# Performance work log

Hardware: AMD Instinct MI355X
Metric: run time of the kernel (lower is better)

The kernel has to match this reference:

```python
import jax, jax.numpy as jnp
import numpy as np

D_MODEL = 1024
N_HEADS = 16
HEAD_DIM = D_MODEL // N_HEADS
B, S = 4, 2048


def setup_inputs() -> dict:
    key = jax.random.key(0)
    ks = jax.random.split(key, 11)
    scale = 1.0 / np.sqrt(D_MODEL)
    inp = {
        "query": jax.random.normal(ks[0], (B, S, D_MODEL), jnp.float32),
        "key": jax.random.normal(ks[1], (B, S, D_MODEL), jnp.float32),
        "value": jax.random.normal(ks[2], (B, S, D_MODEL), jnp.float32),
        "Wq": jax.random.normal(ks[3], (D_MODEL, D_MODEL), jnp.float32) * scale,
        "bq": jnp.zeros((D_MODEL,), jnp.float32),
        "Wk": jax.random.normal(ks[4], (D_MODEL, D_MODEL), jnp.float32) * scale,
        "bk": jnp.zeros((D_MODEL,), jnp.float32),
        "Wv": jax.random.normal(ks[5], (D_MODEL, D_MODEL), jnp.float32) * scale,
        "bv": jnp.zeros((D_MODEL,), jnp.float32),
        "Wo": jax.random.normal(ks[6], (D_MODEL, D_MODEL), jnp.float32) * scale,
        "bo": jnp.zeros((D_MODEL,), jnp.float32),
    }
    return inp


def _split_heads(x):
    b, s, _ = x.shape
    return x.reshape(b, s, N_HEADS, HEAD_DIM).transpose(0, 2, 1, 3)  # b h s d


def reference(query, key, value, Wq, bq, Wk, bk, Wv, bv, Wo, bo):
    Q = _split_heads(query @ Wq.T + bq)
    K = _split_heads(key @ Wk.T + bk)
    V = _split_heads(value @ Wv.T + bv)
    scale = 1.0 / jnp.sqrt(jnp.float32(HEAD_DIM))
    energy = jnp.einsum("bhqd,bhkd->bhqk", Q, K) * scale  # full N x N scores
    attn = jax.nn.softmax(energy, axis=-1)
    x = jnp.einsum("bhqk,bhkd->bhqd", attn, V)
    x = x.transpose(0, 2, 1, 3).reshape(query.shape[0], -1, D_MODEL)
    return x @ Wo.T + bo
```

## Files before the change

### kernel.cpp

```cpp
#include <hip/hip_runtime.h>
#include <cstdint>
#include <cstddef>


typedef unsigned short u16;
typedef unsigned u32;
typedef short short8 __attribute__((ext_vector_type(8)));
typedef __bf16 bf16x8 __attribute__((ext_vector_type(8)));
typedef float f32x4 __attribute__((ext_vector_type(4)));
typedef float f32x16 __attribute__((ext_vector_type(16)));
typedef unsigned short u16x4 __attribute__((ext_vector_type(4)));
typedef unsigned u32x2 __attribute__((ext_vector_type(2)));
typedef unsigned u32x4 __attribute__((ext_vector_type(4)));
typedef int iv2 __attribute__((ext_vector_type(2)));

__device__ __forceinline__ u16 f2bf(float f) {
  unsigned u = __builtin_bit_cast(unsigned, f);
  u += 0x7fffu + ((u >> 16) & 1u);
  return (u16)(u >> 16);
}
__device__ __forceinline__ bf16x8 bc8(short8 v) { return __builtin_bit_cast(bf16x8, v); }
__device__ __forceinline__ u32 pk_bf16(float a, float b) {
  u32 r;
  asm("v_cvt_pk_bf16_f32 %0, %1, %2" : "=v"(r) : "v"(a), "v"(b));
  return r;
}
__device__ __forceinline__ void gload16(const u16* g, u16* l) {
  __builtin_amdgcn_global_load_lds((const __attribute__((address_space(1))) void*)g,
                                   (__attribute__((address_space(3))) void*)l, 16, 0, 0);
}

__global__ __launch_bounds__(256) void cvt_all(const float* __restrict__ q,
                                               const float* __restrict__ k,
                                               const float* __restrict__ v,
                                               const float* __restrict__ wq,
                                               const float* __restrict__ wk,
                                               const float* __restrict__ wv,
                                               const float* __restrict__ wo,
                                               u16* __restrict__ xq, u16* __restrict__ xk,
                                               u16* __restrict__ xv, u16* __restrict__ wqb,
                                               u16* __restrict__ wkb, u16* __restrict__ wvb,
                                               u16* __restrict__ wob) {
  const size_t i4 = (size_t)blockIdx.x * 256 + threadIdx.x;
  const size_t A4 = 1ull << 21, W4 = 1ull << 18;
  const float* s;
  u16* d;
  size_t off;
  if (i4 < 3 * A4) {
    const int r = (int)(i4 >> 21);
    off = i4 & (A4 - 1);
    s = r == 0 ? q : (r == 1 ? k : v);
    d = r == 0 ? xq : (r == 1 ? xk : xv);
  } else {
    const size_t t = i4 - 3 * A4;
    const int r = (int)(t >> 18);
    off = t & (W4 - 1);
    s = r == 0 ? wq : (r == 1 ? wk : (r == 2 ? wv : wo));
    d = r == 0 ? wqb : (r == 1 ? wkb : (r == 2 ? wvb : wob));
  }
  const f32x4 a = ((const f32x4*)s)[off];
  u32x2 o = {pk_bf16(a[0], a[1]), pk_bf16(a[2], a[3])};
  ((u32x2*)d)[off] = o;
}

template <int MODE>
__device__ __forceinline__ void gemm_core(u16* lA, u16* lB,
                                          const u16* __restrict__ A,
                                          const u16* __restrict__ Bw,
                                          const float* __restrict__ bias,
                                          void* __restrict__ C, float oscale,
                                          int M, int N, int K) {
  const int tid = threadIdx.x;
  const int w = tid >> 6, l = tid & 63, g = l >> 4, m = l & 15;
  const int wr = w >> 1, wc = w & 1;
  const int m0 = blockIdx.y * 128, n0 = blockIdx.x * 128;

  const int j0 = w * 2, j1 = w * 2 + 1;
  const int r0 = j0 * 16 + (l >> 2), r1 = j1 * 16 + (l >> 2);
  const int sc8 = (l & 3) * 8;
  const u16* gA0 = A + (size_t)(m0 + r0) * K + sc8;
  const u16* gA1 = A + (size_t)(m0 + r1) * K + sc8;
  const u16* gB0 = Bw + (size_t)(n0 + r0) * K + sc8;
  const u16* gB1 = Bw + (size_t)(n0 + r1) * K + sc8;
  u16* lA0 = lA + j0 * 512;
  u16* lA1 = lA + j1 * 512;
  u16* lB0 = lB + j0 * 512;
  u16* lB1 = lB + j1 * 512;

  f32x4 acc[4][4];
  const f32x4 z = {0.f, 0.f, 0.f, 0.f};
#pragma unroll
  for (int i = 0; i < 4; ++i)
#pragma unroll
    for (int j = 0; j < 4; ++j) acc[i][j] = z;

  const int nk = K >> 5;
  for (int kk = 0; kk < nk; ++kk) {
    const int ko = kk * 32;
    gload16(gA0 + ko, lA0);
    gload16(gA1 + ko, lA1);
    gload16(gB0 + ko, lB0);
    gload16(gB1 + ko, lB1);
    __syncthreads();
    bf16x8 af[4], bf2[4];
#pragma unroll
    for (int i = 0; i < 4; ++i)
      af[i] = bc8(*(const short8*)(lA + (wr * 64 + i * 16 + m) * 32 + g * 8));
#pragma unroll
    for (int j = 0; j < 4; ++j)
      bf2[j] = bc8(*(const short8*)(lB + (wc * 64 + j * 16 + m) * 32 + g * 8));
#pragma unroll
    for (int i = 0; i < 4; ++i)
#pragma unroll
      for (int j = 0; j < 4; ++j)
        acc[i][j] = __builtin_amdgcn_mfma_f32_16x16x32_bf16(af[i], bf2[j], acc[i][j], 0, 0, 0);
    __syncthreads();
  }

  float bv[4];
#pragma unroll
  for (int j = 0; j < 4; ++j) bv[j] = bias[n0 + wc * 64 + j * 16 + m];

  if (MODE == 2) {
#pragma unroll
    for (int i = 0; i < 4; ++i)
#pragma unroll
      for (int j = 0; j < 4; ++j) {
        const int row0 = m0 + wr * 64 + i * 16 + g * 4;
        const int col = n0 + wc * 64 + j * 16 + m;
        u16x4 o;
#pragma unroll
        for (int r = 0; r < 4; ++r) o[r] = f2bf((acc[i][j][r] + bv[j]) * oscale);
        *(u16x4*)((u16*)C + ((size_t)(row0 >> 11) * 1024 + col) * 2048 + (row0 & 2047)) = o;
      }
  } else {
#pragma unroll
    for (int i = 0; i < 4; ++i) {
#pragma unroll
      for (int r = 0; r < 4; ++r) {
        const int row = m0 + wr * 64 + i * 16 + g * 4 + r;
#pragma unroll
        for (int j = 0; j < 4; ++j) {
          const int col = n0 + wc * 64 + j * 16 + m;
          const float v = (acc[i][j][r] + bv[j]) * oscale;
          if (MODE == 0)
            ((float*)C)[(size_t)row * N + col] = v;
          else
            ((u16*)C)[(size_t)row * N + col] = f2bf(v);
        }
      }
    }
  }
}

__global__ __launch_bounds__(256) void qk_gemm(const u16* __restrict__ xq,
                                               const u16* __restrict__ xk,
                                               const u16* __restrict__ wqb,
                                               const u16* __restrict__ wkb,
                                               const float* __restrict__ bq,
                                               const float* __restrict__ bk,
                                               u16* __restrict__ Qp, u16* __restrict__ Kp,
                                               float SC) {
  __shared__ alignas(16) u16 lA[128 * 32];
  __shared__ alignas(16) u16 lB[128 * 32];
  const int z = blockIdx.z;
  gemm_core<1>(lA, lB, z ? xk : xq, z ? wkb : wqb, z ? bk : bq,
               z ? (void*)Kp : (void*)Qp, z ? 1.f : SC, 8192, 1024, 1024);
}

__global__ __launch_bounds__(256) void v_gemm(const u16* __restrict__ xv,
                                              const u16* __restrict__ wvb,
                                              const float* __restrict__ bv,
                                              u16* __restrict__ Vt) {
  __shared__ alignas(16) u16 lA[128 * 32];
  __shared__ alignas(16) u16 lB[128 * 32];
  gemm_core<2>(lA, lB, xv, wvb, bv, Vt, 1.f, 8192, 1024, 1024);
}

__global__ __launch_bounds__(256) void o_gemm(const u16* __restrict__ Xa,
                                              const u16* __restrict__ wob,
                                              const float* __restrict__ bo,
                                              float* __restrict__ out) {
  __shared__ alignas(16) u16 lA[128 * 32];
  __shared__ alignas(16) u16 lB[128 * 32];
  gemm_core<0>(lA, lB, Xa, wob, bo, out, 1.f, 8192, 1024, 1024);
}

__global__ __launch_bounds__(512, 4) void attn_fwd(const u16* __restrict__ Q,
                                                   const u16* __restrict__ Kp,
                                                   const u16* __restrict__ Vt,
                                                   u16* __restrict__ Xa) {
  __shared__ alignas(16) u16 kl[64][72];
  __shared__ alignas(16) u16 vl[64][72];
  const int tid = threadIdx.x;
  const int l = tid & 63, w = tid >> 6;
  const int q32 = l & 31, hi = l >> 5;
  const int lin = blockIdx.x + 8 * blockIdx.y;
  const int xp = lin >> 6, yp = lin & 63;
  const int b = yp >> 4, h = yp & 15;
  const int q0 = xp * 256 + w * 32;

  bf16x8 qf[4];
  const size_t qrow = (size_t)b * 2048 + q0 + q32;
#pragma unroll
  for (int ds = 0; ds < 4; ++ds)
    qf[ds] = bc8(*(const short8*)(Q + qrow * 1024 + h * 64 + ds * 16 + hi * 8));

  f32x16 of[2] = {{}, {}};
  float l0 = 0.f, l1 = 0.f, l2 = 0.f, l3 = 0.f;

  const int sr = tid >> 3;
  const int sc8 = (tid & 7) * 8;
  const u16* Kb = Kp + (size_t)b * 2048 * 1024 + h * 64;
  const u16* Vb = Vt + (size_t)yp * 64 * 2048;

  short8 rk = *(const short8*)(Kb + (size_t)sr * 1024 + sc8);
  short8 rv = *(const short8*)(Vb + (size_t)sr * 2048 + sc8);

  for (int kt = 0; kt < 32; ++kt) {
    *(short8*)(&kl[sr][sc8]) = rk;
    *(short8*)(&vl[sr][sc8]) = rv;
    __syncthreads();
    if (kt + 1 < 32) {
      rk = *(const short8*)(Kb + (size_t)((kt + 1) * 64 + sr) * 1024 + sc8);
      rv = *(const short8*)(Vb + (size_t)sr * 2048 + (kt + 1) * 64 + sc8);
    }

#pragma unroll
    for (int kt2 = 0; kt2 < 2; ++kt2) {
      f32x16 st = {};
#pragma unroll
      for (int ds = 0; ds < 4; ++ds) {
        const bf16x8 kf = bc8(*(const short8*)(&kl[kt2 * 32 + q32][ds * 16 + hi * 8]));
        st = __builtin_amdgcn_mfma_f32_32x32x16_bf16(kf, qf[ds], st, 0, 0, 0);
      }
      float p[16];
#pragma unroll
      for (int r = 0; r < 16; ++r) p[r] = __builtin_amdgcn_exp2f(st[r]);
      l0 += (p[0] + p[1]) + (p[2] + p[3]);
      l1 += (p[4] + p[5]) + (p[6] + p[7]);
      l2 += (p[8] + p[9]) + (p[10] + p[11]);
      l3 += (p[12] + p[13]) + (p[14] + p[15]);
#pragma unroll
      for (int s = 0; s < 2; ++s) {
        int X0 = (int)pk_bf16(p[8 * s + 0], p[8 * s + 1]);
        int X1 = (int)pk_bf16(p[8 * s + 2], p[8 * s + 3]);
        int Y0 = (int)pk_bf16(p[8 * s + 4], p[8 * s + 5]);
        int Y1 = (int)pk_bf16(p[8 * s + 6], p[8 * s + 7]);
        iv2 r0 = __builtin_amdgcn_permlane32_swap(X0, Y0, false, false);
        iv2 r1 = __builtin_amdgcn_permlane32_swap(X1, Y1, false, false);
        u32x4 bw = {(u32)r0[0], (u32)r1[0], (u32)r0[1], (u32)r1[1]};
        const bf16x8 pb = __builtin_bit_cast(bf16x8, bw);
        const int ks = kt2 * 2 + s;
#pragma unroll
        for (int dt = 0; dt < 2; ++dt) {
          const bf16x8 vf = bc8(*(const short8*)(&vl[dt * 32 + q32][ks * 16 + hi * 8]));
          of[dt] = __builtin_amdgcn_mfma_f32_32x32x16_bf16(vf, pb, of[dt], 0, 0, 0);
        }
      }
    }
    __syncthreads();
  }

  float lo = (l0 + l1) + (l2 + l3);
  lo += __shfl_xor(lo, 32, 64);
  const float inv = 1.0f / lo;

#pragma unroll
  for (int dt = 0; dt < 2; ++dt)
#pragma unroll
    for (int rg = 0; rg < 4; ++rg) {
      u32x2 o2;
      o2[0] = pk_bf16(of[dt][4 * rg + 0] * inv, of[dt][4 * rg + 1] * inv);
      o2[1] = pk_bf16(of[dt][4 * rg + 2] * inv, of[dt][4 * rg + 3] * inv);
      *(u32x2*)(Xa + qrow * 1024 + h * 64 + dt * 32 + rg * 8 + hi * 4) = o2;
    }
}

extern "C" void kernel_launch(void* const* d_in, const int* in_sizes, int n_in,
                              void* d_out, int out_size, void* d_ws, size_t ws_size,
                              hipStream_t stream) {
  const float* q  = (const float*)d_in[0];
  const float* k  = (const float*)d_in[1];
  const float* v  = (const float*)d_in[2];
  const float* Wq = (const float*)d_in[3];
  const float* bq = (const float*)d_in[4];
  const float* Wk = (const float*)d_in[5];
  const float* bk = (const float*)d_in[6];
  const float* Wv = (const float*)d_in[7];
  const float* bv = (const float*)d_in[8];
  const float* Wo = (const float*)d_in[9];
  const float* bo = (const float*)d_in[10];

  char* ws = (char*)d_ws;
  const size_t MB = 1024ull * 1024ull;
  u16* wqb = (u16*)(ws + 0 * MB);
  u16* wkb = (u16*)(ws + 2 * MB);
  u16* wvb = (u16*)(ws + 4 * MB);
  u16* wob = (u16*)(ws + 6 * MB);
  u16* xq  = (u16*)(ws + 8 * MB);
  u16* xk  = (u16*)(ws + 24 * MB);
  u16* xv  = (u16*)(ws + 40 * MB);
  u16* Qp  = (u16*)(ws + 56 * MB);
  u16* Kp  = (u16*)(ws + 72 * MB);
  u16* Vt  = xk;
  u16* Xa  = xq;

  cvt_all<<<28672, 256, 0, stream>>>(q, k, v, Wq, Wk, Wv, Wo,
                                     xq, xk, xv, wqb, wkb, wvb, wob);

  const float SC = 0.125f * 1.44269504f;
  qk_gemm<<<dim3(8, 64, 2), 256, 0, stream>>>(xq, xk, wqb, wkb, bq, bk, Qp, Kp, SC);
  v_gemm<<<dim3(8, 64), 256, 0, stream>>>(xv, wvb, bv, Vt);

  attn_fwd<<<dim3(8, 64), 512, 0, stream>>>(Qp, Kp, Vt, Xa);

  o_gemm<<<dim3(8, 64), 256, 0, stream>>>(Xa, wob, bo, (float*)d_out);
}
```

Measured before the change: 224.8 us.

## Fuse fp32-to-bf16 activation conversion into QKV projection GEMM loads

Drops the separate pass that converted the q/k/v activations to bf16. The projection GEMM now loads fp32 tiles straight into LDS using an XOR-swizzled layout and packs them to bf16 while reading fragments. The Q, K and V projections are merged into one launch with a z dimension of 3, and block indices are remapped to group tiles. This removes one full write and re-read of the 48MB activation buffers and one launch, at the cost of twice the A-tile global/LDS traffic inside the GEMM plus conversion ALU work in the inner loop.

```diff
diff --git a/kernel.cpp b/kernel.cpp
--- a/kernel.cpp
+++ b/kernel.cpp
@@ -29,63 +29,68 @@
   __builtin_amdgcn_global_load_lds((const __attribute__((address_space(1))) void*)g,
                                    (__attribute__((address_space(3))) void*)l, 16, 0, 0);
 }
-
-__global__ __launch_bounds__(256) void cvt_all(const float* __restrict__ q,
-                                               const float* __restrict__ k,
-                                               const float* __restrict__ v,
-                                               const float* __restrict__ wq,
-                                               const float* __restrict__ wk,
-                                               const float* __restrict__ wv,
-                                               const float* __restrict__ wo,
-                                               u16* __restrict__ xq, u16* __restrict__ xk,
-                                               u16* __restrict__ xv, u16* __restrict__ wqb,
-                                               u16* __restrict__ wkb, u16* __restrict__ wvb,
-                                               u16* __restrict__ wob) {
+__device__ __forceinline__ void gload16f(const float* g, float* l) {
+  __builtin_amdgcn_global_load_lds((const __attribute__((address_space(1))) void*)g,
+                                   (__attribute__((address_space(3))) void*)l, 16, 0, 0);
+}
+
+__global__ __launch_bounds__(256) void cvt_w(const float* __restrict__ wq,
+                                             const float* __restrict__ wk,
+                                             const float* __restrict__ wv,
+                                             const float* __restrict__ wo,
+                                             u16* __restrict__ wqb, u16* __restrict__ wkb,
+                                             u16* __restrict__ wvb, u16* __restrict__ wob) {
   const size_t i4 = (size_t)blockIdx.x * 256 + threadIdx.x;
-  const size_t A4 = 1ull << 21, W4 = 1ull << 18;
-  const float* s;
-  u16* d;
-  size_t off;
-  if (i4 < 3 * A4) {
-    const int r = (int)(i4 >> 21);
-    off = i4 & (A4 - 1);
-    s = r == 0 ? q : (r == 1 ? k : v);
-    d = r == 0 ? xq : (r == 1 ? xk : xv);
-  } else {
-    const size_t t = i4 - 3 * A4;
-    const int r = (int)(t >> 18);
-    off = t & (W4 - 1);
-    s = r == 0 ? wq : (r == 1 ? wk : (r == 2 ? wv : wo));
-    d = r == 0 ? wqb : (r == 1 ? wkb : (r == 2 ? wvb : wob));
-  }
+  const size_t W4 = 1ull << 18;
+  const int r = (int)(i4 >> 18);
+  const size_t off = i4 & (W4 - 1);
+  const float* s = r == 0 ? wq : (r == 1 ? wk : (r == 2 ? wv : wo));
+  u16* d = r == 0 ? wqb : (r == 1 ? wkb : (r == 2 ? wvb : wob));
   const f32x4 a = ((const f32x4*)s)[off];
   u32x2 o = {pk_bf16(a[0], a[1]), pk_bf16(a[2], a[3])};
   ((u32x2*)d)[off] = o;
 }
 
-template <int MODE>
-__device__ __forceinline__ void gemm_core(u16* lA, u16* lB,
-                                          const u16* __restrict__ A,
+template <int AF32>
+__device__ __forceinline__ void gemm_core(char* lds, const void* __restrict__ A,
                                           const u16* __restrict__ Bw,
                                           const float* __restrict__ bias,
-                                          void* __restrict__ C, float oscale,
-                                          int M, int N, int K) {
+                                          void* __restrict__ C, int mode, float oscale) {
+  constexpr int K = 1024, N = 1024;
   const int tid = threadIdx.x;
   const int w = tid >> 6, l = tid & 63, g = l >> 4, m = l & 15;
   const int wr = w >> 1, wc = w & 1;
-  const int m0 = blockIdx.y * 128, n0 = blockIdx.x * 128;
+  const int lin = blockIdx.x + 8 * blockIdx.y;
+  const int xp = lin >> 6, yp = lin & 63;
+  const int m0 = yp * 128, n0 = xp * 128;
+
+  float* lAf = (float*)lds;
+  u16* lA = (u16*)lds;
+  u16* lB = (u16*)(lds + (AF32 ? 16384 : 8192));
 
   const int j0 = w * 2, j1 = w * 2 + 1;
-  const int r0 = j0 * 16 + (l >> 2), r1 = j1 * 16 + (l >> 2);
-  const int sc8 = (l & 3) * 8;
-  const u16* gA0 = A + (size_t)(m0 + r0) * K + sc8;
-  const u16* gA1 = A + (size_t)(m0 + r1) * K + sc8;
-  const u16* gB0 = Bw + (size_t)(n0 + r0) * K + sc8;
-  const u16* gB1 = Bw + (size_t)(n0 + r1) * K + sc8;
-  u16* lA0 = lA + j0 * 512;
-  u16* lA1 = lA + j1 * 512;
-  u16* lB0 = lB + j0 * 512;
-  u16* lB1 = lB + j1 * 512;
+  const int br0 = j0 * 16 + (l >> 2), br1 = j1 * 16 + (l >> 2);
+  const int bcol = (l & 3) * 8;
+  const u16* gB0 = Bw + (size_t)(n0 + br0) * K + bcol;
+  const u16* gB1 = Bw + (size_t)(n0 + br1) * K + bcol;
+
+  const u16 *gA0 = nullptr, *gA1 = nullptr;
+  const float* gAf[4];
+  float* lAd[4];
+  if constexpr (AF32) {
+    const float* Af = (const float*)A;
+    const int acol = ((l & 7) ^ (l >> 3)) * 4;
+#pragma unroll
+    for (int cc = 0; cc < 4; ++cc) {
+      const int c = w * 4 + cc;
+      gAf[cc] = Af + (size_t)(m0 + c * 8 + (l >> 3)) * K + acol;
+      lAd[cc] = lAf + c * 256;
+    }
+  } else {
+    const u16* Ab = (const u16*)A;
+    gA0 = Ab + (size_t)(m0 + br0) * K + bcol;
+    gA1 = Ab + (size_t)(m0 + br1) * K + bcol;
+  }
 
   f32x4 acc[4][4];
   const f32x4 z = {0.f, 0.f, 0.f, 0.f};
@@ -94,26 +99,43 @@
 #pragma unroll
     for (int j = 0; j < 4; ++j) acc[i][j] = z;
 
-  const int nk = K >> 5;
-  for (int kk = 0; kk < nk; ++kk) {
+  for (int kk = 0; kk < 32; ++kk) {
     const int ko = kk * 32;
-    gload16(gA0 + ko, lA0);
-    gload16(gA1 + ko, lA1);
-    gload16(gB0 + ko, lB0);
-    gload16(gB1 + ko, lB1);
+    if constexpr (AF32) {
+#pragma unroll
+      for (int cc = 0; cc < 4; ++cc) gload16f(gAf[cc] + ko, lAd[cc]);
+    } else {
+      gload16(gA0 + ko, lA + j0 * 512);
+      gload16(gA1 + ko, lA + j1 * 512);
+    }
+    gload16(gB0 + ko, lB + j0 * 512);
+    gload16(gB1 + ko, lB + j1 * 512);
     __syncthreads();
-    bf16x8 af[4], bf2[4];
+
+    bf16x8 af[4], bfr[4];
+#pragma unroll
+    for (int i = 0; i < 4; ++i) {
+      if constexpr (AF32) {
+        const int base = (wr * 64 + i * 16 + m) * 32;
+        const int G0 = ((2 * g) ^ (m & 7)) * 4;
+        const int G1 = ((2 * g + 1) ^ (m & 7)) * 4;
+        const f32x4 lo = *(const f32x4*)(lAf + base + G0);
+        const f32x4 hi = *(const f32x4*)(lAf + base + G1);
+        u32x4 wd = {pk_bf16(lo[0], lo[1]), pk_bf16(lo[2], lo[3]),
+                    pk_bf16(hi[0], hi[1]), pk_bf16(hi[2], hi[3])};
+        af[i] = __builtin_bit_cast(bf16x8, wd);
+      } else {
+        af[i] = bc8(*(const short8*)(lA + (wr * 64 + i * 16 + m) * 32 + g * 8));
+      }
+    }
+#pragma unroll
+    for (int j = 0; j < 4; ++j)
+      bfr[j] = bc8(*(const short8*)(lB + (wc * 64 + j * 16 + m) * 32 + g * 8));
 #pragma unroll
     for (int i = 0; i < 4; ++i)
-      af[i] = bc8(*(const short8*)(lA + (wr * 64 + i * 16 + m) * 32 + g * 8));
-#pragma unroll
-    for (int j = 0; j < 4; ++j)
-      bf2[j] = bc8(*(const short8*)(lB + (wc * 64 + j * 16 + m) * 32 + g * 8));
-#pragma unroll
-    for (int i = 0; i < 4; ++i)
 #pragma unroll
       for (int j = 0; j < 4; ++j)
-        acc[i][j] = __builtin_amdgcn_mfma_f32_16x16x32_bf16(af[i], bf2[j], acc[i][j], 0, 0, 0);
+        acc[i][j] = __builtin_amdgcn_mfma_f32_16x16x32_bf16(af[i], bfr[j], acc[i][j], 0, 0, 0);
     __syncthreads();
   }
 
@@ -121,7 +143,7 @@
 #pragma unroll
   for (int j = 0; j < 4; ++j) bv[j] = bias[n0 + wc * 64 + j * 16 + m];
 
-  if (MODE == 2) {
+  if (mode == 2) {
 #pragma unroll
     for (int i = 0; i < 4; ++i)
 #pragma unroll
@@ -143,7 +165,7 @@
         for (int j = 0; j < 4; ++j) {
           const int col = n0 + wc * 64 + j * 16 + m;
           const float v = (acc[i][j][r] + bv[j]) * oscale;
-          if (MODE == 0)
+          if (mode == 0)
             ((float*)C)[(size_t)row * N + col] = v;
           else
             ((u16*)C)[(size_t)row * N + col] = f2bf(v);
@@ -153,37 +175,32 @@
   }
 }
 
-__global__ __launch_bounds__(256) void qk_gemm(const u16* __restrict__ xq,
-                                               const u16* __restrict__ xk,
-                                               const u16* __restrict__ wqb,
-                                               const u16* __restrict__ wkb,
-                                               const float* __restrict__ bq,
-                                               const float* __restrict__ bk,
-                                               u16* __restrict__ Qp, u16* __restrict__ Kp,
-                                               float SC) {
-  __shared__ alignas(16) u16 lA[128 * 32];
-  __shared__ alignas(16) u16 lB[128 * 32];
+__global__ __launch_bounds__(256) void qkv_gemm(const float* __restrict__ q,
+                                                const float* __restrict__ k,
+                                                const float* __restrict__ v,
+                                                const u16* __restrict__ wqb,
+                                                const u16* __restrict__ wkb,
+                                                const u16* __restrict__ wvb,
+                                                const float* __restrict__ bq,
+                                                const float* __restrict__ bk,
+                                                const float* __restrict__ bv,
+                                                u16* __restrict__ Qp, u16* __restrict__ Kp,
+                                                u16* __restrict__ Vt, float SC) {
+  __shared__ alignas(16) char lds[24576];
   const int z = blockIdx.z;
-  gemm_core<1>(lA, lB, z ? xk : xq, z ? wkb : wqb, z ? bk : bq,
-               z ? (void*)Kp : (void*)Qp, z ? 1.f : SC, 8192, 1024, 1024);
-}
-
-__global__ __launch_bounds__(256) void v_gemm(const u16* __restrict__ xv,
-                                              const u16* __restrict__ wvb,
-                                              const float* __restrict__ bv,
-                                              u16* __restrict__ Vt) {
-  __shared__ alignas(16) u16 lA[128 * 32];
-  __shared__ alignas(16) u16 lB[128 * 32];
-  gemm_core<2>(lA, lB, xv, wvb, bv, Vt, 1.f, 8192, 1024, 1024);
+  const float* A = z == 0 ? q : (z == 1 ? k : v);
+  const u16* W = z == 0 ? wqb : (z == 1 ? wkb : wvb);
+  const float* bi = z == 0 ? bq : (z == 1 ? bk : bv);
+  void* C = z == 0 ? (void*)Qp : (z == 1 ? (void*)Kp : (void*)Vt);
+  gemm_core<1>(lds, A, W, bi, C, z == 2 ? 2 : 1, z == 0 ? SC : 1.f);
 }
 
 __global__ __launch_bounds__(256) void o_gemm(const u16* __restrict__ Xa,
                                               const u16* __restrict__ wob,
                                               const float* __restrict__ bo,
                                               float* __restrict__ out) {
-  __shared__ alignas(16) u16 lA[128 * 32];
-  __shared__ alignas(16) u16 lB[128 * 32];
-  gemm_core<0>(lA, lB, Xa, wob, bo, out, 1.f, 8192, 1024, 1024);
+  __shared__ alignas(16) char lds[16384];
+  gemm_core<0>(lds, Xa, wob, bo, out, 0, 1.f);
 }
 
 __global__ __launch_bounds__(512, 4) void attn_fwd(const u16* __restrict__ Q,
@@ -298,20 +315,16 @@
   u16* wkb = (u16*)(ws + 2 * MB);
   u16* wvb = (u16*)(ws + 4 * MB);
   u16* wob = (u16*)(ws + 6 * MB);
-  u16* xq  = (u16*)(ws + 8 * MB);
-  u16* xk  = (u16*)(ws + 24 * MB);
-  u16* xv  = (u16*)(ws + 40 * MB);
-  u16* Qp  = (u16*)(ws + 56 * MB);
-  u16* Kp  = (u16*)(ws + 72 * MB);
-  u16* Vt  = xk;
-  u16* Xa  = xq;
-
-  cvt_all<<<28672, 256, 0, stream>>>(q, k, v, Wq, Wk, Wv, Wo,
-                                     xq, xk, xv, wqb, wkb, wvb, wob);
+  u16* Qp  = (u16*)(ws + 8 * MB);
+  u16* Kp  = (u16*)(ws + 24 * MB);
+  u16* Vt  = (u16*)(ws + 40 * MB);
+  u16* Xa  = (u16*)(ws + 56 * MB);
+
+  cvt_w<<<4096, 256, 0, stream>>>(Wq, Wk, Wv, Wo, wqb, wkb, wvb, wob);
 
   const float SC = 0.125f * 1.44269504f;
-  qk_gemm<<<dim3(8, 64, 2), 256, 0, stream>>>(xq, xk, wqb, wkb, bq, bk, Qp, Kp, SC);
-  v_gemm<<<dim3(8, 64), 256, 0, stream>>>(xv, wvb, bv, Vt);
+  qkv_gemm<<<dim3(8, 64, 3), 256, 0, stream>>>(q, k, v, wqb, wkb, wvb,
+                                               bq, bk, bv, Qp, Kp, Vt, SC);
 
   attn_fwd<<<dim3(8, 64), 512, 0, stream>>>(Qp, Kp, Vt, Xa);
 
```

New measurement: 230.1 us. 2.4% more time.

## Double-buffer GEMM LDS, use 512-thread blocks, fuse QKV projections into one launch

Applied to the files above, without the earlier changes.

The projection GEMM core now keeps two LDS stages, so the global-to-LDS load for the next K slice is issued before the MFMAs on the current slice. That removes one barrier per iteration and overlaps memory with compute. Blocks grow to 8 waves, each computing a 32x64 sub-tile, and block indices are remapped so that consecutive blocks share row tiles for better L2 reuse. The Q, K and V GEMMs merge into one launch with z=3, and Vt moves to its own workspace region so it no longer aliases xk, which the same launch still reads. The cost is a larger LDS footprint and less register-level reuse per wave.

```diff
diff --git a/kernel.cpp b/kernel.cpp
--- a/kernel.cpp
+++ b/kernel.cpp
@@ -63,57 +63,57 @@
   ((u32x2*)d)[off] = o;
 }
 
-template <int MODE>
-__device__ __forceinline__ void gemm_core(u16* lA, u16* lB,
-                                          const u16* __restrict__ A,
+__device__ __forceinline__ void gemm_core(u16* lds, const u16* __restrict__ A,
                                           const u16* __restrict__ Bw,
                                           const float* __restrict__ bias,
-                                          void* __restrict__ C, float oscale,
-                                          int M, int N, int K) {
+                                          void* __restrict__ C, int mode, float oscale) {
+  constexpr int K = 1024, N = 1024;
   const int tid = threadIdx.x;
   const int w = tid >> 6, l = tid & 63, g = l >> 4, m = l & 15;
-  const int wr = w >> 1, wc = w & 1;
-  const int m0 = blockIdx.y * 128, n0 = blockIdx.x * 128;
-
-  const int j0 = w * 2, j1 = w * 2 + 1;
-  const int r0 = j0 * 16 + (l >> 2), r1 = j1 * 16 + (l >> 2);
-  const int sc8 = (l & 3) * 8;
-  const u16* gA0 = A + (size_t)(m0 + r0) * K + sc8;
-  const u16* gA1 = A + (size_t)(m0 + r1) * K + sc8;
-  const u16* gB0 = Bw + (size_t)(n0 + r0) * K + sc8;
-  const u16* gB1 = Bw + (size_t)(n0 + r1) * K + sc8;
-  u16* lA0 = lA + j0 * 512;
-  u16* lA1 = lA + j1 * 512;
-  u16* lB0 = lB + j0 * 512;
-  u16* lB1 = lB + j1 * 512;
-
-  f32x4 acc[4][4];
+  const int wr = w & 3, wc = w >> 2;
+  const int lin = blockIdx.x + 8 * blockIdx.y;
+  const int xp = lin >> 6, yp = lin & 63;
+  const int m0 = yp * 128, n0 = xp * 128;
+
+  const int srow = w * 16 + (l >> 2);
+  const int scol = (l & 3) * 8;
+  const u16* gA = A + (size_t)(m0 + srow) * K + scol;
+  const u16* gB = Bw + (size_t)(n0 + srow) * K + scol;
+  u16* lA[2] = {lds + 0, lds + 8192};
+  u16* lB[2] = {lds + 4096, lds + 12288};
+  u16* dstA[2] = {lA[0] + w * 512, lA[1] + w * 512};
+  u16* dstB[2] = {lB[0] + w * 512, lB[1] + w * 512};
+
+  f32x4 acc[2][4];
   const f32x4 z = {0.f, 0.f, 0.f, 0.f};
 #pragma unroll
-  for (int i = 0; i < 4; ++i)
+  for (int i = 0; i < 2; ++i)
 #pragma unroll
     for (int j = 0; j < 4; ++j) acc[i][j] = z;
 
-  const int nk = K >> 5;
-  for (int kk = 0; kk < nk; ++kk) {
-    const int ko = kk * 32;
-    gload16(gA0 + ko, lA0);
-    gload16(gA1 + ko, lA1);
-    gload16(gB0 + ko, lB0);
-    gload16(gB1 + ko, lB1);
-    __syncthreads();
-    bf16x8 af[4], bf2[4];
-#pragma unroll
-    for (int i = 0; i < 4; ++i)
-      af[i] = bc8(*(const short8*)(lA + (wr * 64 + i * 16 + m) * 32 + g * 8));
+  gload16(gA, dstA[0]);
+  gload16(gB, dstB[0]);
+  __syncthreads();
+
+  for (int kk = 0; kk < 32; ++kk) {
+    const int cur = kk & 1, nxt = cur ^ 1;
+    if (kk + 1 < 32) {
+      const int ko = (kk + 1) * 32;
+      gload16(gA + ko, dstA[nxt]);
+      gload16(gB + ko, dstB[nxt]);
+    }
+    bf16x8 af[2], bfr[4];
+#pragma unroll
+    for (int i = 0; i < 2; ++i)
+      af[i] = bc8(*(const short8*)(lA[cur] + (wr * 32 + i * 16 + m) * 32 + g * 8));
 #pragma unroll
     for (int j = 0; j < 4; ++j)
-      bf2[j] = bc8(*(const short8*)(lB + (wc * 64 + j * 16 + m) * 32 + g * 8));
-#pragma unroll
-    for (int i = 0; i < 4; ++i)
+      bfr[j] = bc8(*(const short8*)(lB[cur] + (wc * 64 + j * 16 + m) * 32 + g * 8));
+#pragma unroll
+    for (int i = 0; i < 2; ++i)
 #pragma unroll
       for (int j = 0; j < 4; ++j)
-        acc[i][j] = __builtin_amdgcn_mfma_f32_16x16x32_bf16(af[i], bf2[j], acc[i][j], 0, 0, 0);
+        acc[i][j] = __builtin_amdgcn_mfma_f32_16x16x32_bf16(af[i], bfr[j], acc[i][j], 0, 0, 0);
     __syncthreads();
   }
 
@@ -121,12 +121,12 @@
 #pragma unroll
   for (int j = 0; j < 4; ++j) bv[j] = bias[n0 + wc * 64 + j * 16 + m];
 
-  if (MODE == 2) {
-#pragma unroll
-    for (int i = 0; i < 4; ++i)
+  if (mode == 2) {
+#pragma unroll
+    for (int i = 0; i < 2; ++i)
 #pragma unroll
       for (int j = 0; j < 4; ++j) {
-        const int row0 = m0 + wr * 64 + i * 16 + g * 4;
+        const int row0 = m0 + wr * 32 + i * 16 + g * 4;
         const int col = n0 + wc * 64 + j * 16 + m;
         u16x4 o;
 #pragma unroll
@@ -135,15 +135,15 @@
       }
   } else {
 #pragma unroll
-    for (int i = 0; i < 4; ++i) {
+    for (int i = 0; i < 2; ++i) {
 #pragma unroll
       for (int r = 0; r < 4; ++r) {
-        const int row = m0 + wr * 64 + i * 16 + g * 4 + r;
+        const int row = m0 + wr * 32 + i * 16 + g * 4 + r;
 #pragma unroll
         for (int j = 0; j < 4; ++j) {
           const int col = n0 + wc * 64 + j * 16 + m;
           const float v = (acc[i][j][r] + bv[j]) * oscale;
-          if (MODE == 0)
+          if (mode == 0)
             ((float*)C)[(size_t)row * N + col] = v;
           else
             ((u16*)C)[(size_t)row * N + col] = f2bf(v);
@@ -153,37 +153,32 @@
   }
 }
 
-__global__ __launch_bounds__(256) void qk_gemm(const u16* __restrict__ xq,
-                                               const u16* __restrict__ xk,
-                                               const u16* __restrict__ wqb,
-                                               const u16* __restrict__ wkb,
-                                               const float* __restrict__ bq,
-                                               const float* __restrict__ bk,
-                                               u16* __restrict__ Qp, u16* __restrict__ Kp,
-                                               float SC) {
-  __shared__ alignas(16) u16 lA[128 * 32];
-  __shared__ alignas(16) u16 lB[128 * 32];
+__global__ __launch_bounds__(512, 2) void qkv_gemm(const u16* __restrict__ xq,
+                                                   const u16* __restrict__ xk,
+                                                   const u16* __restrict__ xv,
+                                                   const u16* __restrict__ wqb,
+                                                   const u16* __restrict__ wkb,
+                                                   const u16* __restrict__ wvb,
+                                                   const float* __restrict__ bq,
+                                                   const float* __restrict__ bk,
+                                                   const float* __restrict__ bv,
+                                                   u16* __restrict__ Qp, u16* __restrict__ Kp,
+                                                   u16* __restrict__ Vt, float SC) {
+  __shared__ alignas(16) u16 lds[16384];
   const int z = blockIdx.z;
-  gemm_core<1>(lA, lB, z ? xk : xq, z ? wkb : wqb, z ? bk : bq,
-               z ? (void*)Kp : (void*)Qp, z ? 1.f : SC, 8192, 1024, 1024);
-}
-
-__global__ __launch_bounds__(256) void v_gemm(const u16* __restrict__ xv,
-                                              const u16* __restrict__ wvb,
-                                              const float* __restrict__ bv,
-                                              u16* __restrict__ Vt) {
-  __shared__ alignas(16) u16 lA[128 * 32];
-  __shared__ alignas(16) u16 lB[128 * 32];
-  gemm_core<2>(lA, lB, xv, wvb, bv, Vt, 1.f, 8192, 1024, 1024);
-}
-
-__global__ __launch_bounds__(256) void o_gemm(const u16* __restrict__ Xa,
-                                              const u16* __restrict__ wob,
-                                              const float* __restrict__ bo,
-                                              float* __restrict__ out) {
-  __shared__ alignas(16) u16 lA[128 * 32];
-  __shared__ alignas(16) u16 lB[128 * 32];
-  gemm_core<0>(lA, lB, Xa, wob, bo, out, 1.f, 8192, 1024, 1024);
+  const u16* A = z == 0 ? xq : (z == 1 ? xk : xv);
+  const u16* W = z == 0 ? wqb : (z == 1 ? wkb : wvb);
+  const float* bi = z == 0 ? bq : (z == 1 ? bk : bv);
+  void* C = z == 0 ? (void*)Qp : (z == 1 ? (void*)Kp : (void*)Vt);
+  gemm_core(lds, A, W, bi, C, z == 2 ? 2 : 1, z == 0 ? SC : 1.f);
+}
+
+__global__ __launch_bounds__(512, 2) void o_gemm(const u16* __restrict__ Xa,
+                                                 const u16* __restrict__ wob,
+                                                 const float* __restrict__ bo,
+                                                 float* __restrict__ out) {
+  __shared__ alignas(16) u16 lds[16384];
+  gemm_core(lds, Xa, wob, bo, out, 0, 1.f);
 }
 
 __global__ __launch_bounds__(512, 4) void attn_fwd(const u16* __restrict__ Q,
@@ -306,14 +301,16 @@
   u16* Vt  = xk;
   u16* Xa  = xq;
 
+  Vt = (u16*)(ws + 88 * MB);
+
   cvt_all<<<28672, 256, 0, stream>>>(q, k, v, Wq, Wk, Wv, Wo,
                                      xq, xk, xv, wqb, wkb, wvb, wob);
 
   const float SC = 0.125f * 1.44269504f;
-  qk_gemm<<<dim3(8, 64, 2), 256, 0, stream>>>(xq, xk, wqb, wkb, bq, bk, Qp, Kp, SC);
-  v_gemm<<<dim3(8, 64), 256, 0, stream>>>(xv, wvb, bv, Vt);
+  qkv_gemm<<<dim3(8, 64, 3), 512, 0, stream>>>(xq, xk, xv, wqb, wkb, wvb,
+                                               bq, bk, bv, Qp, Kp, Vt, SC);
 
   attn_fwd<<<dim3(8, 64), 512, 0, stream>>>(Qp, Kp, Vt, Xa);
 
-  o_gemm<<<dim3(8, 64), 256, 0, stream>>>(Xa, wob, bo, (float*)d_out);
-}
+  o_gemm<<<dim3(8, 64), 512, 0, stream>>>(Xa, wob, bo, (float*)d_out);
+}
```

Result: slower. 255.1 us (+13.5%).
